# Performance work log

Measured on AMD Instinct MI355X. Metric: run time of the kernel, lower is better.

Reference implementation:

```python
import jax, jax.numpy as jnp
import numpy as np
import math

B = 8192          # per_replica_batch_size
D = 256           # embedding_dim
R = 8             # num_relations
N = 1024          # in_batch_negatives
F = 2             # embedding features per node (summed)


def setup_inputs() -> dict:
    key = jax.random.key(0)
    k_emb, k_tr = jax.random.split(key)
    emb = jax.random.normal(k_emb, (2 * B, F, D), dtype=jnp.float32)
    trans_embs = jax.random.uniform(k_tr, (R, D), dtype=jnp.float32)
    # relations: equal count per relation so shapes are static under jit
    rels_np = (np.arange(B) % R).astype(np.int32)
    order_np = np.argsort(rels_np, kind='stable').astype(np.int32)  # rows grouped by relation
    rng = np.random.default_rng(0)
    C = B // R
    reps = math.ceil(N / C)
    neg_lhs = np.empty((R, N), dtype=np.int32)
    neg_rhs = np.empty((R, N), dtype=np.int32)
    for r in range(R):  # small fixed loop over relations, host-side only
        rows = np.where(rels_np == r)[0]
        neg_lhs[r] = rows[np.tile(rng.permutation(C), reps)[:N]]
        neg_rhs[r] = rows[np.tile(rng.permutation(C), reps)[:N]]
    return {
        'emb': emb,
        'trans_embs': trans_embs,
        'rels': jnp.asarray(rels_np),
        'order': jnp.asarray(order_np),
        'neg_lhs_idx': jnp.asarray(neg_lhs),
        'neg_rhs_idx': jnp.asarray(neg_rhs),
    }


def reference(emb, trans_embs, rels, order, neg_lhs_idx, neg_rhs_idx):
    b = rels.shape[0]
    d = emb.shape[-1]
    r, n = neg_lhs_idx.shape
    c = b // r
    # sum feature embeddings per node, split into (lhs, rhs) pairs
    x = jnp.sum(emb, axis=1).reshape(b, 2, d)
    lhs = x[:, 0, :]
    rhs = x[:, 1, :]
    translated = rhs + trans_embs[rels]
    pos = jnp.sum(lhs * translated, axis=-1)  # [B]
    # relation-grouped rows (stable original order within each relation)
    s_lhs = lhs[order].reshape(r, c, d)
    s_rhs = rhs[order].reshape(r, c, d)
    samp_lhs = lhs[neg_lhs_idx]  # [R, N, D]
    samp_rhs = rhs[neg_rhs_idx]  # [R, N, D]
    # negs_lhs = rhs_matrix @ sampled_lhs.T ; negs_rhs = lhs_matrix @ sampled_rhs.T
    negs_lhs = jnp.einsum('rcd,rnd->rcn', s_rhs, samp_lhs).reshape(r, c * n)
    negs_rhs = jnp.einsum('rcd,rnd->rcn', s_lhs, samp_rhs).reshape(r, c * n)
    # per relation: [negs_lhs_flat, negs_rhs_flat], concatenated over relations
    negs = jnp.concatenate([negs_lhs, negs_rhs], axis=1).reshape(-1)
    logits = jnp.concatenate([pos, negs])
    return logits, jax.nn.sigmoid(logits)
```

## Files before the change

### kernel.cpp

```cpp
#include <hip/hip_runtime.h>
#include <hip/hip_bf16.h>
#include <stdint.h>

#define B_SZ 8192
#define D_SZ 256
#define R_SZ 8
#define N_SZ 1024
#define C_SZ (B_SZ / R_SZ)
#define CN   (C_SZ * N_SZ)
#define L_SZ (B_SZ + 2 * R_SZ * CN)

#define FP_SCALE 1792.0f
#define FP_INV_S2 3.113918e-7f

typedef int   i32x4 __attribute__((ext_vector_type(4)));
typedef float f32x4 __attribute__((ext_vector_type(4)));

static __device__ __forceinline__ float sigmoidf_(float x) {
  return 1.0f / (1.0f + __expf(-x));
}
static __device__ __forceinline__ void gload16(const void* g, void* l) {
  __builtin_amdgcn_global_load_lds(
      (const __attribute__((address_space(1))) void*)g,
      (__attribute__((address_space(3))) void*)l, 16, 0, 0);
}


__global__ __launch_bounds__(256) void prep_kernel(
    const float* __restrict__ emb, const float* __restrict__ trans,
    const int* __restrict__ rels, float* __restrict__ out,
    char* __restrict__ ws) {
  char* lhs_H = ws;
  char* lhs_L = ws + ((size_t)2 << 20);
  char* rhs_H = ws + ((size_t)4 << 20);
  char* rhs_L = ws + ((size_t)6 << 20);

  int wave = threadIdx.x >> 6;
  int lane = threadIdx.x & 63;
  int i = blockIdx.x * 4 + wave;

  const float4* emb4 = (const float4*)emb;
  size_t bl = (size_t)(2 * i) * 128;
  size_t br = (size_t)(2 * i + 1) * 128;
  float4 a0 = emb4[bl + lane];
  float4 a1 = emb4[bl + 64 + lane];
  float4 b0 = emb4[br + lane];
  float4 b1 = emb4[br + 64 + lane];
  float lh[4] = {a0.x + a1.x, a0.y + a1.y, a0.z + a1.z, a0.w + a1.w};
  float rh[4] = {b0.x + b1.x, b0.y + b1.y, b0.z + b1.z, b0.w + b1.w};

  int rel = rels[i];
  float4 tv = ((const float4*)trans)[rel * 64 + lane];
  float tt[4] = {tv.x, tv.y, tv.z, tv.w};

  float p = 0.f;
#pragma unroll
  for (int j = 0; j < 4; ++j) p += lh[j] * (rh[j] + tt[j]);
#pragma unroll
  for (int off = 32; off; off >>= 1) p += __shfl_xor(p, off, 64);
  if (lane == 0) {
    out[i] = p;
    out[(size_t)L_SZ + i] = sigmoidf_(p);
  }

  int phL = 0, plL = 0, phR = 0, plR = 0;
#pragma unroll
  for (int j = 0; j < 4; ++j) {
    float t = fminf(fmaxf(lh[j] * FP_SCALE, -16256.f), 16256.f);
    int hi = __float2int_rn(t * 0.0078125f);
    int lo = __float2int_rn(t) - (hi << 7);
    phL |= (hi & 255) << (8 * j);
    plL |= (lo & 255) << (8 * j);
    t = fminf(fmaxf(rh[j] * FP_SCALE, -16256.f), 16256.f);
    hi = __float2int_rn(t * 0.0078125f);
    lo = __float2int_rn(t) - (hi << 7);
    phR |= (hi & 255) << (8 * j);
    plR |= (lo & 255) << (8 * j);
  }
  size_t rowb = (size_t)i * 256 + lane * 4;
  *(int*)(lhs_H + rowb) = phL;
  *(int*)(lhs_L + rowb) = plL;
  *(int*)(rhs_H + rowb) = phR;
  *(int*)(rhs_L + rowb) = plR;
}

__global__ __launch_bounds__(256, 4) void negs_kernel(
    const char* __restrict__ ws,
    const int* __restrict__ order,
    const int* __restrict__ negL, const int* __restrict__ negR,
    float* __restrict__ out) {
  __shared__ char lds[2][16384];

  const char* lhs_H = ws;
  const char* lhs_L = ws + ((size_t)2 << 20);
  const char* rhs_H = ws + ((size_t)4 << 20);
  const char* rhs_L = ws + ((size_t)6 << 20);

  int hw = blockIdx.x;
  int bid = (hw & 7) * 512 + (hw >> 3);
  int ntile = bid & 15;
  int ctile = (bid >> 4) & 15;
  int side  = (bid >> 8) & 1;
  int r     = bid >> 9;

  int wave = threadIdx.x >> 6;
  int lane = threadIdx.x & 63;
  int wrow = wave >> 1, wcol = wave & 1;
  int lx = lane & 15;
  int q = lane >> 4;

  const char* srcp;
  const int* idxp;
  int idxbase;
  if (wave < 2) {
    idxp = order;
    idxbase = r * C_SZ + ctile * 64;
    srcp = (wave == 0) ? (side ? lhs_H : rhs_H) : (side ? lhs_L : rhs_L);
  } else {
    idxp = side ? negR : negL;
    idxbase = r * N_SZ + ntile * 64;
    srcp = (wave == 2) ? (side ? rhs_H : lhs_H) : (side ? rhs_L : lhs_L);
  }
  int myoff = wave * 4096;

  unsigned srcswz = (unsigned)(((lane & 3) ^ ((lane >> 3) & 3)) << 4);
  unsigned goff[4];
#pragma unroll
  for (int it = 0; it < 4; ++it) {
    int grow = idxp[idxbase + it * 16 + (lane >> 2)];
    goff[it] = (unsigned)grow * 256u + srcswz;
  }

  i32x4 acc1[2][2] = {};
  i32x4 acc2[2][2] = {};

#pragma unroll
  for (int it = 0; it < 4; ++it)
    gload16(srcp + goff[it], &lds[0][myoff] + it * 1024);
  __syncthreads();

#pragma unroll 1
  for (int kc = 0; kc < 4; ++kc) {
    if (kc < 3) {
      char* nl = &lds[(kc + 1) & 1][myoff];
#pragma unroll
      for (int it = 0; it < 4; ++it)
        gload16(srcp + goff[it] + (unsigned)(kc + 1) * 64u, nl + it * 1024);
    }

    const char* L0 = &lds[kc & 1][0];
    i32x4 ha[2], la[2], hb[2], lb[2];
#pragma unroll
    for (int mi = 0; mi < 2; ++mi) {
      int row = wrow * 32 + mi * 16 + lx;
      int off = row * 64 + ((q ^ ((row >> 1) & 3)) << 4);
      ha[mi] = *(const i32x4*)(L0 + off);
      la[mi] = *(const i32x4*)(L0 + 4096 + off);
    }
#pragma unroll
    for (int ni = 0; ni < 2; ++ni) {
      int row = wcol * 32 + ni * 16 + lx;
      int off = row * 64 + ((q ^ ((row >> 1) & 3)) << 4);
      hb[ni] = *(const i32x4*)(L0 + 8192 + off);
      lb[ni] = *(const i32x4*)(L0 + 12288 + off);
    }
#pragma unroll
    for (int mi = 0; mi < 2; ++mi)
#pragma unroll
      for (int ni = 0; ni < 2; ++ni) {
        acc1[mi][ni] = __builtin_amdgcn_mfma_i32_16x16x64_i8(ha[mi], hb[ni], acc1[mi][ni], 0, 0, 0);
        acc2[mi][ni] = __builtin_amdgcn_mfma_i32_16x16x64_i8(la[mi], hb[ni], acc2[mi][ni], 0, 0, 0);
        acc2[mi][ni] = __builtin_amdgcn_mfma_i32_16x16x64_i8(ha[mi], lb[ni], acc2[mi][ni], 0, 0, 0);
      }

    __syncthreads();
  }

  size_t obase = (size_t)B_SZ + ((size_t)(r * 2 + side)) * CN;
  int gcb = ntile * 64 + wcol * 32 + lx;
  int grb = ctile * 64 + wrow * 32 + ((lane >> 4) << 2);
#pragma unroll
  for (int mi = 0; mi < 2; ++mi) {
#pragma unroll
    for (int jj = 0; jj < 4; ++jj) {
      int gr = grb + mi * 16 + jj;
      size_t rowb = obase + (size_t)gr * N_SZ;
      float v[2], s[2];
#pragma unroll
      for (int ni = 0; ni < 2; ++ni) {
        v[ni] = fmaf(16384.0f, (float)acc1[mi][ni][jj],
                     128.0f * (float)acc2[mi][ni][jj]) * FP_INV_S2;
        s[ni] = sigmoidf_(v[ni]);
      }
#pragma unroll
      for (int ni = 0; ni < 2; ++ni)
        out[rowb + gcb + ni * 16] = v[ni];
#pragma unroll
      for (int ni = 0; ni < 2; ++ni)
        out[(size_t)L_SZ + rowb + gcb + ni * 16] = s[ni];
    }
  }
}

extern "C" void kernel_launch(void* const* d_in, const int* in_sizes, int n_in,
                              void* d_out, int out_size, void* d_ws, size_t ws_size,
                              hipStream_t stream) {
  const float* emb   = (const float*)d_in[0];
  const float* trans = (const float*)d_in[1];
  const int*   rels  = (const int*)d_in[2];
  const int*   order = (const int*)d_in[3];
  const int*   negL  = (const int*)d_in[4];
  const int*   negR  = (const int*)d_in[5];
  float* out = (float*)d_out;
  char* ws = (char*)d_ws;

  prep_kernel<<<B_SZ / 4, 256, 0, stream>>>(emb, trans, rels, out, ws);
  negs_kernel<<<4096, 256, 0, stream>>>(ws, order, negL, negR, out);
}
```

Before: 42.57 us.

## Loop each negs block over four N-tiles and map relations to XCDs

Each negs block now processes four consecutive 64-column N-tiles in sequence rather than one, and the grid shrinks from 4096 to 1024 blocks. The block-to-work mapping is changed so that relation r lands on XCD r, keeping each relation's data in one L2. The next N-tile's gather is issued before the current tile's epilogue stores so the loads can overlap the output writes. In exchange, the A-side rows are still re-gathered for every N-tile, and fewer blocks may reduce the latency hiding available across the GPU.

Measured after the change: 44.12 us. +3.6%, slower.

```diff
diff --git a/kernel.cpp b/kernel.cpp
--- a/kernel.cpp
+++ b/kernel.cpp
@@ -96,12 +96,12 @@
   const char* rhs_H = ws + ((size_t)4 << 20);
   const char* rhs_L = ws + ((size_t)6 << 20);
 
-  int hw = blockIdx.x;
-  int bid = (hw & 7) * 512 + (hw >> 3);
-  int ntile = bid & 15;
-  int ctile = (bid >> 4) & 15;
-  int side  = (bid >> 8) & 1;
-  int r     = bid >> 9;
+  int p = blockIdx.x;
+  int xcd = p & 7, pin = p >> 3;
+  int r     = xcd;
+  int side  = (pin >> 6) & 1;
+  int ctile = (pin >> 2) & 15;
+  int nt0   = (pin & 3) * 4;
 
   int wave = threadIdx.x >> 6;
   int lane = threadIdx.x & 63;
@@ -111,28 +111,24 @@
 
   const char* srcp;
   const int* idxp;
-  int idxbase;
   if (wave < 2) {
     idxp = order;
-    idxbase = r * C_SZ + ctile * 64;
     srcp = (wave == 0) ? (side ? lhs_H : rhs_H) : (side ? lhs_L : rhs_L);
   } else {
     idxp = side ? negR : negL;
-    idxbase = r * N_SZ + ntile * 64;
     srcp = (wave == 2) ? (side ? rhs_H : lhs_H) : (side ? rhs_L : lhs_L);
   }
   int myoff = wave * 4096;
 
   unsigned srcswz = (unsigned)(((lane & 3) ^ ((lane >> 3) & 3)) << 4);
+
   unsigned goff[4];
-#pragma unroll
-  for (int it = 0; it < 4; ++it) {
-    int grow = idxp[idxbase + it * 16 + (lane >> 2)];
-    goff[it] = (unsigned)grow * 256u + srcswz;
-  }
-
-  i32x4 acc1[2][2] = {};
-  i32x4 acc2[2][2] = {};
+  {
+    int base = (wave < 2) ? (r * C_SZ + ctile * 64) : (r * N_SZ + nt0 * 64);
+#pragma unroll
+    for (int it = 0; it < 4; ++it)
+      goff[it] = (unsigned)idxp[base + it * 16 + (lane >> 2)] * 256u + srcswz;
+  }
 
 #pragma unroll
   for (int it = 0; it < 4; ++it)
@@ -140,65 +136,85 @@
   __syncthreads();
 
 #pragma unroll 1
-  for (int kc = 0; kc < 4; ++kc) {
-    if (kc < 3) {
-      char* nl = &lds[(kc + 1) & 1][myoff];
+  for (int tk = 0; tk < 4; ++tk) {
+    i32x4 acc1[2][2] = {};
+    i32x4 acc2[2][2] = {};
+
+#pragma unroll 1
+    for (int kc = 0; kc < 4; ++kc) {
+      if (kc < 3) {
+        char* nl = &lds[(kc + 1) & 1][myoff];
+#pragma unroll
+        for (int it = 0; it < 4; ++it)
+          gload16(srcp + goff[it] + (unsigned)(kc + 1) * 64u, nl + it * 1024);
+      }
+
+      const char* L0 = &lds[kc & 1][0];
+      i32x4 ha[2], la[2], hb[2], lb[2];
+#pragma unroll
+      for (int mi = 0; mi < 2; ++mi) {
+        int row = wrow * 32 + mi * 16 + lx;
+        int off = row * 64 + ((q ^ ((row >> 1) & 3)) << 4);
+        ha[mi] = *(const i32x4*)(L0 + off);
+        la[mi] = *(const i32x4*)(L0 + 4096 + off);
+      }
+#pragma unroll
+      for (int ni = 0; ni < 2; ++ni) {
+        int row = wcol * 32 + ni * 16 + lx;
+        int off = row * 64 + ((q ^ ((row >> 1) & 3)) << 4);
+        hb[ni] = *(const i32x4*)(L0 + 8192 + off);
+        lb[ni] = *(const i32x4*)(L0 + 12288 + off);
+      }
+#pragma unroll
+      for (int mi = 0; mi < 2; ++mi)
+#pragma unroll
+        for (int ni = 0; ni < 2; ++ni) {
+          acc1[mi][ni] = __builtin_amdgcn_mfma_i32_16x16x64_i8(ha[mi], hb[ni], acc1[mi][ni], 0, 0, 0);
+          acc2[mi][ni] = __builtin_amdgcn_mfma_i32_16x16x64_i8(la[mi], hb[ni], acc2[mi][ni], 0, 0, 0);
+          acc2[mi][ni] = __builtin_amdgcn_mfma_i32_16x16x64_i8(ha[mi], lb[ni], acc2[mi][ni], 0, 0, 0);
+        }
+
+      __syncthreads();
+    }
+    if (tk < 3) {
+      if (wave >= 2) {
+        int base = r * N_SZ + (nt0 + tk + 1) * 64;
+#pragma unroll
+        for (int it = 0; it < 4; ++it)
+          goff[it] = (unsigned)idxp[base + it * 16 + (lane >> 2)] * 256u + srcswz;
+      }
 #pragma unroll
       for (int it = 0; it < 4; ++it)
-        gload16(srcp + goff[it] + (unsigned)(kc + 1) * 64u, nl + it * 1024);
+        gload16(srcp + goff[it], &lds[0][myoff] + it * 1024);
     }
 
-    const char* L0 = &lds[kc & 1][0];
-    i32x4 ha[2], la[2], hb[2], lb[2];
+    int ntile = nt0 + tk;
+    size_t obase = (size_t)B_SZ + ((size_t)(r * 2 + side)) * CN;
+    int gcb = ntile * 64 + wcol * 32 + lx;
+    int grb = ctile * 64 + wrow * 32 + ((lane >> 4) << 2);
 #pragma unroll
     for (int mi = 0; mi < 2; ++mi) {
-      int row = wrow * 32 + mi * 16 + lx;
-      int off = row * 64 + ((q ^ ((row >> 1) & 3)) << 4);
-      ha[mi] = *(const i32x4*)(L0 + off);
-      la[mi] = *(const i32x4*)(L0 + 4096 + off);
+#pragma unroll
+      for (int jj = 0; jj < 4; ++jj) {
+        int gr = grb + mi * 16 + jj;
+        size_t rowb = obase + (size_t)gr * N_SZ;
+        float v[2], s[2];
+#pragma unroll
+        for (int ni = 0; ni < 2; ++ni) {
+          v[ni] = fmaf(16384.0f, (float)acc1[mi][ni][jj],
+                       128.0f * (float)acc2[mi][ni][jj]) * FP_INV_S2;
+          s[ni] = sigmoidf_(v[ni]);
+        }
+#pragma unroll
+        for (int ni = 0; ni < 2; ++ni)
+          out[rowb + gcb + ni * 16] = v[ni];
+#pragma unroll
+        for (int ni = 0; ni < 2; ++ni)
+          out[(size_t)L_SZ + rowb + gcb + ni * 16] = s[ni];
+      }
     }
-#pragma unroll
-    for (int ni = 0; ni < 2; ++ni) {
-      int row = wcol * 32 + ni * 16 + lx;
-      int off = row * 64 + ((q ^ ((row >> 1) & 3)) << 4);
-      hb[ni] = *(const i32x4*)(L0 + 8192 + off);
-      lb[ni] = *(const i32x4*)(L0 + 12288 + off);
-    }
-#pragma unroll
-    for (int mi = 0; mi < 2; ++mi)
-#pragma unroll
-      for (int ni = 0; ni < 2; ++ni) {
-        acc1[mi][ni] = __builtin_amdgcn_mfma_i32_16x16x64_i8(ha[mi], hb[ni], acc1[mi][ni], 0, 0, 0);
-        acc2[mi][ni] = __builtin_amdgcn_mfma_i32_16x16x64_i8(la[mi], hb[ni], acc2[mi][ni], 0, 0, 0);
-        acc2[mi][ni] = __builtin_amdgcn_mfma_i32_16x16x64_i8(ha[mi], lb[ni], acc2[mi][ni], 0, 0, 0);
-      }
-
-    __syncthreads();
-  }
-
-  size_t obase = (size_t)B_SZ + ((size_t)(r * 2 + side)) * CN;
-  int gcb = ntile * 64 + wcol * 32 + lx;
-  int grb = ctile * 64 + wrow * 32 + ((lane >> 4) << 2);
-#pragma unroll
-  for (int mi = 0; mi < 2; ++mi) {
-#pragma unroll
-    for (int jj = 0; jj < 4; ++jj) {
-      int gr = grb + mi * 16 + jj;
-      size_t rowb = obase + (size_t)gr * N_SZ;
-      float v[2], s[2];
-#pragma unroll
-      for (int ni = 0; ni < 2; ++ni) {
-        v[ni] = fmaf(16384.0f, (float)acc1[mi][ni][jj],
-                     128.0f * (float)acc2[mi][ni][jj]) * FP_INV_S2;
-        s[ni] = sigmoidf_(v[ni]);
-      }
-#pragma unroll
-      for (int ni = 0; ni < 2; ++ni)
-        out[rowb + gcb + ni * 16] = v[ni];
-#pragma unroll
-      for (int ni = 0; ni < 2; ++ni)
-        out[(size_t)L_SZ + rowb + gcb + ni * 16] = s[ni];
-    }
+
+    if (tk < 3) __syncthreads();
   }
 }
 
@@ -215,5 +231,5 @@
   char* ws = (char*)d_ws;
 
   prep_kernel<<<B_SZ / 4, 256, 0, stream>>>(emb, trans, rels, out, ws);
-  negs_kernel<<<4096, 256, 0, stream>>>(ws, order, negL, negR, out);
-}
+  negs_kernel<<<1024, 256, 0, stream>>>(ws, order, negL, negR, out);
+}
```
